# Performance work log

Hardware: AMD Instinct MI355X
Metric: run time of the kernel (lower is better)

Reference implementation:

```python
import jax, jax.numpy as jnp
import numpy as np

H = 64   # hidden_layers
D = 1    # frame_dimension
N = 2048 # n_samples (batch)
T = 512  # seq_len


def setup_inputs() -> dict:
    key = jax.random.key(0)
    ks = jax.random.split(key, 12)
    s = 1.0 / np.sqrt(H)
    u = lambda k, shape: jax.random.uniform(k, shape, jnp.float32, -s, s)
    return {
        "y": jax.random.normal(ks[0], (N, T), dtype=jnp.float32),
        "W_ih1": u(ks[1], (4 * H, D)),
        "W_hh1": u(ks[2], (4 * H, H)),
        "b_ih1": u(ks[3], (4 * H,)),
        "b_hh1": u(ks[4], (4 * H,)),
        "W_ih2": u(ks[5], (4 * H, H)),
        "W_hh2": u(ks[6], (4 * H, H)),
        "b_ih2": u(ks[7], (4 * H,)),
        "b_hh2": u(ks[8], (4 * H,)),
        "W_lin": u(ks[9], (D, H)),
        "b_lin": u(ks[10], (D,)),
        "pre_output_len": 1,
    }


def _lstm_cell(x, h, c, W_ih, W_hh, b_ih, b_hh):
    # gates in PyTorch LSTMCell order: input, forget, cell(g), output
    g = x @ W_ih.T + b_ih + h @ W_hh.T + b_hh  # [n, 4H]
    i, f, gg, o = jnp.split(g, 4, axis=-1)
    i = jax.nn.sigmoid(i)
    f = jax.nn.sigmoid(f)
    gg = jnp.tanh(gg)
    o = jax.nn.sigmoid(o)
    c2 = f * c + i * gg
    h2 = o * jnp.tanh(c2)
    return h2, c2


def reference(y, W_ih1, W_hh1, b_ih1, b_hh1, W_ih2, W_hh2, b_ih2, b_hh2,
              W_lin, b_lin, pre_output_len):
    n = y.shape[0]
    zeros = jnp.zeros((n, H), dtype=jnp.float32)
    init = (zeros, zeros, zeros, zeros)

    def step(carry, x_t):
        h1, c1, h2, c2 = carry
        h1, c1 = _lstm_cell(x_t, h1, c1, W_ih1, W_hh1, b_ih1, b_hh1)
        h2, c2 = _lstm_cell(h1, h2, c2, W_ih2, W_hh2, b_ih2, b_hh2)
        out = h2 @ W_lin.T + b_lin  # [n, D]
        return (h1, c1, h2, c2), out

    ys = jnp.swapaxes(y, 0, 1)[:, :, None]  # [T, n, 1]
    _, outs = jax.lax.scan(step, init, ys)  # [T, n, D]
    outs = outs[pre_output_len:]            # drop first pre_output_len steps (static)
    # torch.cat along dim=1 of [n, D] chunks -> [n, (T - pre)*D]
    return jnp.transpose(outs, (1, 0, 2)).reshape(n, -1)
```

## Files before the change

### kernel.cpp

```cpp
#include <hip/hip_runtime.h>


typedef __attribute__((ext_vector_type(8))) short short8;
typedef __attribute__((ext_vector_type(4))) float f32x4;

#define XPITCH 2060
#define XP 0
#define HP 32960
#define OPR 51392
#define LDS_BYTES 84160
#define PLANE(layer, buf, hl) (HP + ((((layer) * 2 + (buf)) * 2) + (hl)) * 2304)

__device__ __forceinline__ float fast_rcp(float x) { return __builtin_amdgcn_rcpf(x); }
__device__ __forceinline__ float sigm(float x) { return fast_rcp(1.0f + __expf(-x)); }
__device__ __forceinline__ float tanh2(float x) {
  const float e = __expf(-2.0f * x);
  return fmaf(2.0f, fast_rcp(1.0f + e), -1.0f);
}
__device__ __forceinline__ unsigned short bf_rne(float f) {
  unsigned u = __float_as_uint(f);
  return (unsigned short)((u + 0x7FFFu + ((u >> 16) & 1u)) >> 16);
}
__device__ __forceinline__ void split8(const float* p, short8& hi, short8& lo) {
#pragma unroll
  for (int e = 0; e < 8; ++e) {
    float v = p[e];
    unsigned short h = bf_rne(v);
    float hf = __uint_as_float(((unsigned)h) << 16);
    hi[e] = (short)h;
    lo[e] = (short)bf_rne(v - hf);
  }
}
__device__ __forceinline__ unsigned cvt_pk(float a, float b) {
  unsigned r;
  asm("v_cvt_pk_bf16_f32 %0, %1, %2" : "=v"(r) : "v"(a), "v"(b));
  return r;
}
__device__ __forceinline__ f32x4 mfma16(short8 a, short8 b, f32x4 c) {
  return __builtin_amdgcn_mfma_f32_16x16x32_bf16(a, b, c, 0, 0, 0);
}

__global__ __launch_bounds__(512, 2) void lstm2_pipe(
    const float* __restrict__ y, const float* __restrict__ Wih1,
    const float* __restrict__ Whh1, const float* __restrict__ bih1,
    const float* __restrict__ bhh1, const float* __restrict__ Wih2,
    const float* __restrict__ Whh2, const float* __restrict__ bih2,
    const float* __restrict__ bhh2, const float* __restrict__ Wlin,
    const float* __restrict__ blin, float* __restrict__ out) {
  extern __shared__ char smem[];
  const int tid = threadIdx.x;
  const int w = tid >> 6;
  const int lane = tid & 63;
  const int g = lane >> 4;
  const int s = lane & 15;
  const int s0 = blockIdx.x * 16;

  for (int i = tid; i < 16 * 512; i += 512) {
    const int ss = i >> 9, t = i & 511;
    *(float*)(smem + XP + ss * XPITCH + t * 4) = y[(size_t)(s0 + ss) * 512 + t];
  }
  for (int i = tid; i < 18432 / 4; i += 512) *(float*)(smem + HP + i * 4) = 0.f;

  const float bl0 = blin[0];
  __syncthreads();

  if (w < 4) {
    short8 a1h[4][2], a1l[4][2];
    {
      const int row = 16 * w + s;
#pragma unroll
      for (int p = 0; p < 4; ++p)
#pragma unroll
        for (int c = 0; c < 2; ++c)
          split8(Whh1 + (size_t)(p * 64 + row) * 64 + 32 * c + 8 * g, a1h[p][c], a1l[p][c]);
    }
    float bias1c[4][4], wih1c[4][4];
#pragma unroll
    for (int p = 0; p < 4; ++p)
#pragma unroll
      for (int r = 0; r < 4; ++r) {
        const int row = p * 64 + 16 * w + 4 * g + r;
        bias1c[p][r] = bih1[row] + bhh1[row];
        wih1c[p][r] = Wih1[row];
      }
    float c1[4] = {0.f, 0.f, 0.f, 0.f};
    const int boffc0 = s * 144 + 16 * g;
    const int hoff = s * 144 + 32 * w + 8 * g;

#pragma unroll 1
    for (int k = 0; k <= 512; ++k) {
      if (k < 512) {
        const int rbuf = (k - 1) & 1;
        const int wbuf = k & 1;
        const float x = *(const float*)(smem + XP + s * XPITCH + k * 4);
        f32x4 acc[4];
#pragma unroll
        for (int p = 0; p < 4; ++p)
#pragma unroll
          for (int r = 0; r < 4; ++r) acc[p][r] = fmaf(wih1c[p][r], x, bias1c[p][r]);
#pragma unroll
        for (int c = 0; c < 2; ++c) {
          const int boff = boffc0 + 64 * c;
          const short8 Bh = *(const short8*)(smem + PLANE(0, rbuf, 0) + boff);
          const short8 Bl = *(const short8*)(smem + PLANE(0, rbuf, 1) + boff);
#pragma unroll
          for (int p = 0; p < 4; ++p) acc[p] = mfma16(a1h[p][c], Bh, acc[p]);
#pragma unroll
          for (int p = 0; p < 4; ++p) acc[p] = mfma16(a1h[p][c], Bl, acc[p]);
#pragma unroll
          for (int p = 0; p < 4; ++p) acc[p] = mfma16(a1l[p][c], Bh, acc[p]);
        }
        float h1n[4];
#pragma unroll
        for (int r = 0; r < 4; ++r) {
          const float ig = sigm(acc[0][r]), fg = sigm(acc[1][r]);
          const float gg = tanh2(acc[2][r]), og = sigm(acc[3][r]);
          c1[r] = fmaf(fg, c1[r], ig * gg);
          h1n[r] = og * tanh2(c1[r]);
        }
        const unsigned hA = cvt_pk(h1n[0], h1n[1]), hB = cvt_pk(h1n[2], h1n[3]);
        const unsigned lA = cvt_pk(h1n[0] - __uint_as_float(hA << 16),
                                   h1n[1] - __uint_as_float(hA & 0xFFFF0000u));
        const unsigned lB = cvt_pk(h1n[2] - __uint_as_float(hB << 16),
                                   h1n[3] - __uint_as_float(hB & 0xFFFF0000u));
        *(uint2*)(smem + PLANE(0, wbuf, 0) + hoff) = make_uint2(hA, hB);
        *(uint2*)(smem + PLANE(0, wbuf, 1) + hoff) = make_uint2(lA, lB);
      }
      __syncthreads();
    }
  } else {
    const int ow = w - 4;
    short8 a2h[4][4], a2l[4][4];
    {
      const int row = 16 * ow + s;
#pragma unroll
      for (int p = 0; p < 4; ++p)
#pragma unroll
        for (int c = 0; c < 4; ++c) {
          const float* src = (c < 2) ? (Wih2 + (size_t)(p * 64 + row) * 64 + 32 * c + 8 * g)
                                     : (Whh2 + (size_t)(p * 64 + row) * 64 + 32 * (c - 2) + 8 * g);
          split8(src, a2h[p][c], a2l[p][c]);
        }
    }
    float bias2c[4][4], wlinc[4];
#pragma unroll
    for (int p = 0; p < 4; ++p)
#pragma unroll
      for (int r = 0; r < 4; ++r) {
        const int row = p * 64 + 16 * ow + 4 * g + r;
        bias2c[p][r] = bih2[row] + bhh2[row];
      }
#pragma unroll
    for (int r = 0; r < 4; ++r) wlinc[r] = Wlin[16 * ow + 4 * g + r];
    float c2[4] = {0.f, 0.f, 0.f, 0.f};
    const int boffc0 = s * 144 + 16 * g;
    const int hoff = s * 144 + 32 * ow + 8 * g;

#pragma unroll 1
    for (int k = 0; k <= 512; ++k) {
      if (k >= 66 && ((k - 2) & 63) == 0) {
        const int base = k - 66;
        const int thr = ow * 64 + lane;
        const int ss = thr & 15, grp = thr >> 4;
#pragma unroll
        for (int q = 0; q < 4; ++q) {
          const int idx = base + grp * 4 + q;
          const int slot = idx & 127;
          const char* op = smem + OPR + slot * 256 + ss * 4;
          const float v = *(const float*)(op) + *(const float*)(op + 64) +
                          *(const float*)(op + 128) + *(const float*)(op + 192) + bl0;
          out[(size_t)(s0 + ss) * 511 + idx] = v;
        }
      }
      if (k >= 1) {
        const int t2 = k - 1;
        const int h1buf = (k - 1) & 1;
        const int h2rbuf = k & 1;
        const int h2wbuf = (k - 1) & 1;
        f32x4 acc[4];
#pragma unroll
        for (int p = 0; p < 4; ++p)
#pragma unroll
          for (int r = 0; r < 4; ++r) acc[p][r] = bias2c[p][r];
#pragma unroll
        for (int c = 0; c < 4; ++c) {
          const int lay = (c < 2) ? 0 : 1;
          const int buf = (c < 2) ? h1buf : h2rbuf;
          const int boff = boffc0 + 64 * (c & 1);
          const short8 Bh = *(const short8*)(smem + PLANE(lay, buf, 0) + boff);
          const short8 Bl = *(const short8*)(smem + PLANE(lay, buf, 1) + boff);
#pragma unroll
          for (int p = 0; p < 4; ++p) acc[p] = mfma16(a2h[p][c], Bh, acc[p]);
#pragma unroll
          for (int p = 0; p < 4; ++p) acc[p] = mfma16(a2h[p][c], Bl, acc[p]);
#pragma unroll
          for (int p = 0; p < 4; ++p) acc[p] = mfma16(a2l[p][c], Bh, acc[p]);
        }
        float h2n[4];
#pragma unroll
        for (int r = 0; r < 4; ++r) {
          const float ig = sigm(acc[0][r]), fg = sigm(acc[1][r]);
          const float gg = tanh2(acc[2][r]), og = sigm(acc[3][r]);
          c2[r] = fmaf(fg, c2[r], ig * gg);
          h2n[r] = og * tanh2(c2[r]);
        }
        const unsigned hA = cvt_pk(h2n[0], h2n[1]), hB = cvt_pk(h2n[2], h2n[3]);
        const unsigned lA = cvt_pk(h2n[0] - __uint_as_float(hA << 16),
                                   h2n[1] - __uint_as_float(hA & 0xFFFF0000u));
        const unsigned lB = cvt_pk(h2n[2] - __uint_as_float(hB << 16),
                                   h2n[3] - __uint_as_float(hB & 0xFFFF0000u));
        *(uint2*)(smem + PLANE(1, h2wbuf, 0) + hoff) = make_uint2(hA, hB);
        *(uint2*)(smem + PLANE(1, h2wbuf, 1) + hoff) = make_uint2(lA, lB);

        if (t2 >= 1) {
          float pw = wlinc[0] * h2n[0];
          pw = fmaf(wlinc[1], h2n[1], pw);
          pw = fmaf(wlinc[2], h2n[2], pw);
          pw = fmaf(wlinc[3], h2n[3], pw);
          pw += __shfl_xor(pw, 16, 64);
          pw += __shfl_xor(pw, 32, 64);
          if (g == 0)
            *(float*)(smem + OPR + ((t2 - 1) & 127) * 256 + ow * 64 + s * 4) = pw;
        }
      }
      __syncthreads();
    }
    {
      const int thr = ow * 64 + lane;
      for (int e = thr; e < 63 * 16; e += 256) {
        const int ss = e & 15, off = e >> 4;
        const int idx = 448 + off;
        const int slot = idx & 127;
        const char* op = smem + OPR + slot * 256 + ss * 4;
        const float v = *(const float*)(op) + *(const float*)(op + 64) +
                        *(const float*)(op + 128) + *(const float*)(op + 192) + bl0;
        out[(size_t)(s0 + ss) * 511 + idx] = v;
      }
    }
  }
}

extern "C" void kernel_launch(void* const* d_in, const int* in_sizes, int n_in,
                              void* d_out, int out_size, void* d_ws, size_t ws_size,
                              hipStream_t stream) {
  const float* y    = (const float*)d_in[0];
  const float* Wih1 = (const float*)d_in[1];
  const float* Whh1 = (const float*)d_in[2];
  const float* bih1 = (const float*)d_in[3];
  const float* bhh1 = (const float*)d_in[4];
  const float* Wih2 = (const float*)d_in[5];
  const float* Whh2 = (const float*)d_in[6];
  const float* bih2 = (const float*)d_in[7];
  const float* bhh2 = (const float*)d_in[8];
  const float* Wlin = (const float*)d_in[9];
  const float* blin = (const float*)d_in[10];
  float* out = (float*)d_out;

  hipFuncSetAttribute((const void*)lstm2_pipe,
                      hipFuncAttributeMaxDynamicSharedMemorySize, LDS_BYTES);
  lstm2_pipe<<<dim3(128), dim3(512), LDS_BYTES, stream>>>(
      y, Wih1, Whh1, bih1, bhh1, Wih2, Whh2, bih2, bhh2, Wlin, blin, out);
}
```

Baseline: 648.0 us.

## Replace block barriers with LDS flag counters and 4-slot ring for layer decoupling

Replaces the per-step __syncthreads between layer-1 and layer-2 wavegroups with per-wave progress counters in LDS and spin-waits. Hidden states go into a 4-slot ring, so layer 1 can run up to three steps ahead of layer 2. It also splits the MFMA chains into two independent accumulators to shorten dependency latency, raises priority around the MFMA block, and fuses the gate math into fewer exp/rcp calls. The cost is more LDS, spin-wait polling overhead, and the risk of memory-ordering bugs in the flag protocol.

```diff
diff --git a/kernel.cpp b/kernel.cpp
--- a/kernel.cpp
+++ b/kernel.cpp
@@ -4,19 +4,16 @@
 typedef __attribute__((ext_vector_type(8))) short short8;
 typedef __attribute__((ext_vector_type(4))) float f32x4;
 
+#define NT 512
 #define XPITCH 2060
 #define XP 0
 #define HP 32960
-#define OPR 51392
-#define LDS_BYTES 84160
-#define PLANE(layer, buf, hl) (HP + ((((layer) * 2 + (buf)) * 2) + (hl)) * 2304)
+#define RING 69824
+#define FLG 102592
+#define LDS_BYTES 102720
+#define PLANE(layer, slot, hl) (HP + ((((layer) * 4 + (slot)) * 2) + (hl)) * 2304)
 
 __device__ __forceinline__ float fast_rcp(float x) { return __builtin_amdgcn_rcpf(x); }
-__device__ __forceinline__ float sigm(float x) { return fast_rcp(1.0f + __expf(-x)); }
-__device__ __forceinline__ float tanh2(float x) {
-  const float e = __expf(-2.0f * x);
-  return fmaf(2.0f, fast_rcp(1.0f + e), -1.0f);
-}
 __device__ __forceinline__ unsigned short bf_rne(float f) {
   unsigned u = __float_as_uint(f);
   return (unsigned short)((u + 0x7FFFu + ((u >> 16) & 1u)) >> 16);
@@ -39,8 +36,25 @@
 __device__ __forceinline__ f32x4 mfma16(short8 a, short8 b, f32x4 c) {
   return __builtin_amdgcn_mfma_f32_16x16x32_bf16(a, b, c, 0, 0, 0);
 }
-
-__global__ __launch_bounds__(512, 2) void lstm2_pipe(
+__device__ __forceinline__ void cell(float i, float f, float gg, float o,
+                                     float& c, float& h) {
+  const float ei = __expf(-i), ef = __expf(-f), eg = __expf(-2.f * gg),
+              eo = __expf(-o);
+  const float P = (1.f - eg) * fast_rcp((1.f + ei) * (1.f + eg));
+  c = fmaf(c, fast_rcp(1.f + ef), P);
+  const float cc = fminf(15.f, fmaxf(-15.f, c));
+  const float ec = __expf(-2.f * cc);
+  h = (1.f - ec) * fast_rcp((1.f + eo) * (1.f + ec));
+}
+__device__ __forceinline__ void wait_min_ge(const volatile int* c4, int need) {
+  while (true) {
+    const int m = min(min(c4[0], c4[1]), min(c4[2], c4[3]));
+    if (m >= need) return;
+    __builtin_amdgcn_s_sleep(1);
+  }
+}
+
+__global__ __launch_bounds__(512, 2) void lstm2_async(
     const float* __restrict__ y, const float* __restrict__ Wih1,
     const float* __restrict__ Whh1, const float* __restrict__ bih1,
     const float* __restrict__ bhh1, const float* __restrict__ Wih2,
@@ -59,21 +73,22 @@
     const int ss = i >> 9, t = i & 511;
     *(float*)(smem + XP + ss * XPITCH + t * 4) = y[(size_t)(s0 + ss) * 512 + t];
   }
-  for (int i = tid; i < 18432 / 4; i += 512) *(float*)(smem + HP + i * 4) = 0.f;
-
-  const float bl0 = blin[0];
+  for (int i = tid; i < 36864 / 4; i += 512) *(float*)(smem + HP + i * 4) = 0.f;
+  if (tid < 8) *(volatile int*)(smem + FLG + tid * 4) = -1;
   __syncthreads();
+
+  volatile int* cE = (volatile int*)(smem + FLG);
+  volatile int* cO = (volatile int*)(smem + FLG + 16);
+  const int bo0 = s * 144 + 16 * g, bo1 = bo0 + 64;
 
   if (w < 4) {
     short8 a1h[4][2], a1l[4][2];
-    {
-      const int row = 16 * w + s;
-#pragma unroll
-      for (int p = 0; p < 4; ++p)
-#pragma unroll
-        for (int c = 0; c < 2; ++c)
-          split8(Whh1 + (size_t)(p * 64 + row) * 64 + 32 * c + 8 * g, a1h[p][c], a1l[p][c]);
-    }
+#pragma unroll
+    for (int p = 0; p < 4; ++p)
+#pragma unroll
+      for (int c = 0; c < 2; ++c)
+        split8(Whh1 + (size_t)(p * 64 + 16 * w + s) * 64 + 32 * c + 8 * g,
+               a1h[p][c], a1l[p][c]);
     float bias1c[4][4], wih1c[4][4];
 #pragma unroll
     for (int p = 0; p < 4; ++p)
@@ -84,157 +99,183 @@
         wih1c[p][r] = Wih1[row];
       }
     float c1[4] = {0.f, 0.f, 0.f, 0.f};
-    const int boffc0 = s * 144 + 16 * g;
-    const int hoff = s * 144 + 32 * w + 8 * g;
+    const int hwr0 = s * 144 + 32 * w + 8 * g;
 
 #pragma unroll 1
-    for (int k = 0; k <= 512; ++k) {
-      if (k < 512) {
-        const int rbuf = (k - 1) & 1;
-        const int wbuf = k & 1;
-        const float x = *(const float*)(smem + XP + s * XPITCH + k * 4);
-        f32x4 acc[4];
-#pragma unroll
-        for (int p = 0; p < 4; ++p)
-#pragma unroll
-          for (int r = 0; r < 4; ++r) acc[p][r] = fmaf(wih1c[p][r], x, bias1c[p][r]);
-#pragma unroll
-        for (int c = 0; c < 2; ++c) {
-          const int boff = boffc0 + 64 * c;
-          const short8 Bh = *(const short8*)(smem + PLANE(0, rbuf, 0) + boff);
-          const short8 Bl = *(const short8*)(smem + PLANE(0, rbuf, 1) + boff);
-#pragma unroll
-          for (int p = 0; p < 4; ++p) acc[p] = mfma16(a1h[p][c], Bh, acc[p]);
-#pragma unroll
-          for (int p = 0; p < 4; ++p) acc[p] = mfma16(a1h[p][c], Bl, acc[p]);
-#pragma unroll
-          for (int p = 0; p < 4; ++p) acc[p] = mfma16(a1l[p][c], Bh, acc[p]);
-        }
-        float h1n[4];
-#pragma unroll
-        for (int r = 0; r < 4; ++r) {
-          const float ig = sigm(acc[0][r]), fg = sigm(acc[1][r]);
-          const float gg = tanh2(acc[2][r]), og = sigm(acc[3][r]);
-          c1[r] = fmaf(fg, c1[r], ig * gg);
-          h1n[r] = og * tanh2(c1[r]);
-        }
-        const unsigned hA = cvt_pk(h1n[0], h1n[1]), hB = cvt_pk(h1n[2], h1n[3]);
-        const unsigned lA = cvt_pk(h1n[0] - __uint_as_float(hA << 16),
-                                   h1n[1] - __uint_as_float(hA & 0xFFFF0000u));
-        const unsigned lB = cvt_pk(h1n[2] - __uint_as_float(hB << 16),
-                                   h1n[3] - __uint_as_float(hB & 0xFFFF0000u));
-        *(uint2*)(smem + PLANE(0, wbuf, 0) + hoff) = make_uint2(hA, hB);
-        *(uint2*)(smem + PLANE(0, wbuf, 1) + hoff) = make_uint2(lA, lB);
-      }
-      __syncthreads();
+    for (int k = 0; k < NT; ++k) {
+      if (k >= 1) wait_min_ge(cE, k - 1);
+      if (k >= 4) wait_min_ge(cO, k - 4);
+      asm volatile("" ::: "memory");
+      const int rp0 = PLANE(0, (k - 1) & 3, 0), rp1 = PLANE(0, (k - 1) & 3, 1);
+      const short8 Bh0 = *(const short8*)(smem + rp0 + bo0);
+      const short8 Bl0 = *(const short8*)(smem + rp1 + bo0);
+      const short8 Bh1 = *(const short8*)(smem + rp0 + bo1);
+      const short8 Bl1 = *(const short8*)(smem + rp1 + bo1);
+      const float x = *(const float*)(smem + XP + s * XPITCH + k * 4);
+      f32x4 acc[4], acx[4];
+#pragma unroll
+      for (int p = 0; p < 4; ++p) {
+#pragma unroll
+        for (int r = 0; r < 4; ++r) acc[p][r] = fmaf(wih1c[p][r], x, bias1c[p][r]);
+        acx[p] = (f32x4){0.f, 0.f, 0.f, 0.f};
+      }
+      __builtin_amdgcn_s_setprio(1);
+#pragma unroll
+      for (int p = 0; p < 4; ++p) acc[p] = mfma16(a1h[p][0], Bh0, acc[p]);
+#pragma unroll
+      for (int p = 0; p < 4; ++p) acx[p] = mfma16(a1h[p][1], Bh1, acx[p]);
+#pragma unroll
+      for (int p = 0; p < 4; ++p) acc[p] = mfma16(a1h[p][0], Bl0, acc[p]);
+#pragma unroll
+      for (int p = 0; p < 4; ++p) acx[p] = mfma16(a1h[p][1], Bl1, acx[p]);
+#pragma unroll
+      for (int p = 0; p < 4; ++p) acc[p] = mfma16(a1l[p][0], Bh0, acc[p]);
+#pragma unroll
+      for (int p = 0; p < 4; ++p) acx[p] = mfma16(a1l[p][1], Bh1, acx[p]);
+      __builtin_amdgcn_s_setprio(0);
+#pragma unroll
+      for (int p = 0; p < 4; ++p) acc[p] += acx[p];
+
+      float h1n[4];
+#pragma unroll
+      for (int r = 0; r < 4; ++r)
+        cell(acc[0][r], acc[1][r], acc[2][r], acc[3][r], c1[r], h1n[r]);
+      const unsigned hA = cvt_pk(h1n[0], h1n[1]), hB = cvt_pk(h1n[2], h1n[3]);
+      const unsigned lA = cvt_pk(h1n[0] - __uint_as_float(hA << 16),
+                                 h1n[1] - __uint_as_float(hA & 0xFFFF0000u));
+      const unsigned lB = cvt_pk(h1n[2] - __uint_as_float(hB << 16),
+                                 h1n[3] - __uint_as_float(hB & 0xFFFF0000u));
+      *(uint2*)(smem + PLANE(0, k & 3, 0) + hwr0) = make_uint2(hA, hB);
+      *(uint2*)(smem + PLANE(0, k & 3, 1) + hwr0) = make_uint2(lA, lB);
+      asm volatile("s_waitcnt lgkmcnt(0)" ::: "memory");
+      if (lane == 0) cE[w] = k;
     }
   } else {
     const int ow = w - 4;
     short8 a2h[4][4], a2l[4][4];
-    {
-      const int row = 16 * ow + s;
-#pragma unroll
-      for (int p = 0; p < 4; ++p)
-#pragma unroll
-        for (int c = 0; c < 4; ++c) {
-          const float* src = (c < 2) ? (Wih2 + (size_t)(p * 64 + row) * 64 + 32 * c + 8 * g)
-                                     : (Whh2 + (size_t)(p * 64 + row) * 64 + 32 * (c - 2) + 8 * g);
-          split8(src, a2h[p][c], a2l[p][c]);
-        }
-    }
+#pragma unroll
+    for (int p = 0; p < 4; ++p)
+#pragma unroll
+      for (int c = 0; c < 4; ++c) {
+        const float* src = (c < 2) ? (Wih2 + (size_t)(p * 64 + 16 * ow + s) * 64 + 32 * c + 8 * g)
+                                   : (Whh2 + (size_t)(p * 64 + 16 * ow + s) * 64 + 32 * (c - 2) + 8 * g);
+        split8(src, a2h[p][c], a2l[p][c]);
+      }
     float bias2c[4][4], wlinc[4];
 #pragma unroll
     for (int p = 0; p < 4; ++p)
 #pragma unroll
-      for (int r = 0; r < 4; ++r) {
-        const int row = p * 64 + 16 * ow + 4 * g + r;
-        bias2c[p][r] = bih2[row] + bhh2[row];
-      }
+      for (int r = 0; r < 4; ++r)
+        bias2c[p][r] = bih2[p * 64 + 16 * ow + 4 * g + r] +
+                       bhh2[p * 64 + 16 * ow + 4 * g + r];
 #pragma unroll
     for (int r = 0; r < 4; ++r) wlinc[r] = Wlin[16 * ow + 4 * g + r];
+    const float bl0 = blin[0];
     float c2[4] = {0.f, 0.f, 0.f, 0.f};
-    const int boffc0 = s * 144 + 16 * g;
-    const int hoff = s * 144 + 32 * ow + 8 * g;
+    const int hwr0 = s * 144 + 32 * ow + 8 * g;
 
 #pragma unroll 1
-    for (int k = 0; k <= 512; ++k) {
-      if (k >= 66 && ((k - 2) & 63) == 0) {
-        const int base = k - 66;
+    for (int j = 0; j < NT; ++j) {
+      wait_min_ge(cE, j);
+      if (j >= 1) wait_min_ge(cO, j - 1);
+      asm volatile("" ::: "memory");
+
+      if (j >= 66 && ((j - 2) & 63) == 0) {
+        const int base = j - 66;
         const int thr = ow * 64 + lane;
-        const int ss = thr & 15, grp = thr >> 4;
+        const int ss2 = thr & 15, grp = thr >> 4;
 #pragma unroll
         for (int q = 0; q < 4; ++q) {
           const int idx = base + grp * 4 + q;
-          const int slot = idx & 127;
-          const char* op = smem + OPR + slot * 256 + ss * 4;
+          const char* op = smem + RING + (idx & 127) * 256 + ss2 * 4;
           const float v = *(const float*)(op) + *(const float*)(op + 64) +
                           *(const float*)(op + 128) + *(const float*)(op + 192) + bl0;
-          out[(size_t)(s0 + ss) * 511 + idx] = v;
+          out[(size_t)(s0 + ss2) * 511 + idx] = v;
         }
       }
-      if (k >= 1) {
-        const int t2 = k - 1;
-        const int h1buf = (k - 1) & 1;
-        const int h2rbuf = k & 1;
-        const int h2wbuf = (k - 1) & 1;
-        f32x4 acc[4];
-#pragma unroll
-        for (int p = 0; p < 4; ++p)
-#pragma unroll
-          for (int r = 0; r < 4; ++r) acc[p][r] = bias2c[p][r];
-#pragma unroll
-        for (int c = 0; c < 4; ++c) {
-          const int lay = (c < 2) ? 0 : 1;
-          const int buf = (c < 2) ? h1buf : h2rbuf;
-          const int boff = boffc0 + 64 * (c & 1);
-          const short8 Bh = *(const short8*)(smem + PLANE(lay, buf, 0) + boff);
-          const short8 Bl = *(const short8*)(smem + PLANE(lay, buf, 1) + boff);
-#pragma unroll
-          for (int p = 0; p < 4; ++p) acc[p] = mfma16(a2h[p][c], Bh, acc[p]);
-#pragma unroll
-          for (int p = 0; p < 4; ++p) acc[p] = mfma16(a2h[p][c], Bl, acc[p]);
-#pragma unroll
-          for (int p = 0; p < 4; ++p) acc[p] = mfma16(a2l[p][c], Bh, acc[p]);
-        }
-        float h2n[4];
-#pragma unroll
-        for (int r = 0; r < 4; ++r) {
-          const float ig = sigm(acc[0][r]), fg = sigm(acc[1][r]);
-          const float gg = tanh2(acc[2][r]), og = sigm(acc[3][r]);
-          c2[r] = fmaf(fg, c2[r], ig * gg);
-          h2n[r] = og * tanh2(c2[r]);
-        }
-        const unsigned hA = cvt_pk(h2n[0], h2n[1]), hB = cvt_pk(h2n[2], h2n[3]);
-        const unsigned lA = cvt_pk(h2n[0] - __uint_as_float(hA << 16),
-                                   h2n[1] - __uint_as_float(hA & 0xFFFF0000u));
-        const unsigned lB = cvt_pk(h2n[2] - __uint_as_float(hB << 16),
-                                   h2n[3] - __uint_as_float(hB & 0xFFFF0000u));
-        *(uint2*)(smem + PLANE(1, h2wbuf, 0) + hoff) = make_uint2(hA, hB);
-        *(uint2*)(smem + PLANE(1, h2wbuf, 1) + hoff) = make_uint2(lA, lB);
-
-        if (t2 >= 1) {
-          float pw = wlinc[0] * h2n[0];
-          pw = fmaf(wlinc[1], h2n[1], pw);
-          pw = fmaf(wlinc[2], h2n[2], pw);
-          pw = fmaf(wlinc[3], h2n[3], pw);
-          pw += __shfl_xor(pw, 16, 64);
-          pw += __shfl_xor(pw, 32, 64);
-          if (g == 0)
-            *(float*)(smem + OPR + ((t2 - 1) & 127) * 256 + ow * 64 + s * 4) = pw;
-        }
-      }
-      __syncthreads();
+
+      const int rp0 = PLANE(0, j & 3, 0), rp1 = PLANE(0, j & 3, 1);
+      const int rq0 = PLANE(1, (j - 1) & 3, 0), rq1 = PLANE(1, (j - 1) & 3, 1);
+      const short8 Bh0 = *(const short8*)(smem + rp0 + bo0);
+      const short8 Bl0 = *(const short8*)(smem + rp1 + bo0);
+      const short8 Bh1 = *(const short8*)(smem + rp0 + bo1);
+      const short8 Bl1 = *(const short8*)(smem + rp1 + bo1);
+      const short8 Ch0 = *(const short8*)(smem + rq0 + bo0);
+      const short8 Cl0 = *(const short8*)(smem + rq1 + bo0);
+      const short8 Ch1 = *(const short8*)(smem + rq0 + bo1);
+      const short8 Cl1 = *(const short8*)(smem + rq1 + bo1);
+      f32x4 acc[4], acx[4];
+#pragma unroll
+      for (int p = 0; p < 4; ++p) {
+        acc[p] = (f32x4){bias2c[p][0], bias2c[p][1], bias2c[p][2], bias2c[p][3]};
+        acx[p] = (f32x4){0.f, 0.f, 0.f, 0.f};
+      }
+      __builtin_amdgcn_s_setprio(1);
+#pragma unroll
+      for (int p = 0; p < 4; ++p) acc[p] = mfma16(a2h[p][0], Bh0, acc[p]);
+#pragma unroll
+      for (int p = 0; p < 4; ++p) acx[p] = mfma16(a2h[p][1], Bh1, acx[p]);
+#pragma unroll
+      for (int p = 0; p < 4; ++p) acc[p] = mfma16(a2h[p][0], Bl0, acc[p]);
+#pragma unroll
+      for (int p = 0; p < 4; ++p) acx[p] = mfma16(a2h[p][1], Bl1, acx[p]);
+#pragma unroll
+      for (int p = 0; p < 4; ++p) acc[p] = mfma16(a2l[p][0], Bh0, acc[p]);
+#pragma unroll
+      for (int p = 0; p < 4; ++p) acx[p] = mfma16(a2l[p][1], Bh1, acx[p]);
+#pragma unroll
+      for (int p = 0; p < 4; ++p) acc[p] = mfma16(a2h[p][2], Ch0, acc[p]);
+#pragma unroll
+      for (int p = 0; p < 4; ++p) acx[p] = mfma16(a2h[p][3], Ch1, acx[p]);
+#pragma unroll
+      for (int p = 0; p < 4; ++p) acc[p] = mfma16(a2h[p][2], Cl0, acc[p]);
+#pragma unroll
+      for (int p = 0; p < 4; ++p) acx[p] = mfma16(a2h[p][3], Cl1, acx[p]);
+#pragma unroll
+      for (int p = 0; p < 4; ++p) acc[p] = mfma16(a2l[p][2], Ch0, acc[p]);
+#pragma unroll
+      for (int p = 0; p < 4; ++p) acx[p] = mfma16(a2l[p][3], Ch1, acx[p]);
+      __builtin_amdgcn_s_setprio(0);
+#pragma unroll
+      for (int p = 0; p < 4; ++p) acc[p] += acx[p];
+
+      float h2n[4];
+#pragma unroll
+      for (int r = 0; r < 4; ++r)
+        cell(acc[0][r], acc[1][r], acc[2][r], acc[3][r], c2[r], h2n[r]);
+      const unsigned hA = cvt_pk(h2n[0], h2n[1]), hB = cvt_pk(h2n[2], h2n[3]);
+      const unsigned lA = cvt_pk(h2n[0] - __uint_as_float(hA << 16),
+                                 h2n[1] - __uint_as_float(hA & 0xFFFF0000u));
+      const unsigned lB = cvt_pk(h2n[2] - __uint_as_float(hB << 16),
+                                 h2n[3] - __uint_as_float(hB & 0xFFFF0000u));
+      *(uint2*)(smem + PLANE(1, j & 3, 0) + hwr0) = make_uint2(hA, hB);
+      *(uint2*)(smem + PLANE(1, j & 3, 1) + hwr0) = make_uint2(lA, lB);
+
+      if (j >= 1) {
+        float pw = wlinc[0] * h2n[0];
+        pw = fmaf(wlinc[1], h2n[1], pw);
+        pw = fmaf(wlinc[2], h2n[2], pw);
+        pw = fmaf(wlinc[3], h2n[3], pw);
+        pw += __shfl_xor(pw, 16, 64);
+        pw += __shfl_xor(pw, 32, 64);
+        if (g == 0)
+          *(float*)(smem + RING + ((j - 1) & 127) * 256 + ow * 64 + s * 4) = pw;
+      }
+      asm volatile("s_waitcnt lgkmcnt(0)" ::: "memory");
+      if (lane == 0) cO[ow] = j;
     }
+
+    wait_min_ge(cO, NT - 1);
+    asm volatile("" ::: "memory");
     {
       const int thr = ow * 64 + lane;
       for (int e = thr; e < 63 * 16; e += 256) {
-        const int ss = e & 15, off = e >> 4;
+        const int ss2 = e & 15, off = e >> 4;
         const int idx = 448 + off;
-        const int slot = idx & 127;
-        const char* op = smem + OPR + slot * 256 + ss * 4;
+        const char* op = smem + RING + (idx & 127) * 256 + ss2 * 4;
         const float v = *(const float*)(op) + *(const float*)(op + 64) +
                         *(const float*)(op + 128) + *(const float*)(op + 192) + bl0;
-        out[(size_t)(s0 + ss) * 511 + idx] = v;
+        out[(size_t)(s0 + ss2) * 511 + idx] = v;
       }
     }
   }
@@ -256,8 +297,8 @@
   const float* blin = (const float*)d_in[10];
   float* out = (float*)d_out;
 
-  hipFuncSetAttribute((const void*)lstm2_pipe,
+  hipFuncSetAttribute((const void*)lstm2_async,
                       hipFuncAttributeMaxDynamicSharedMemorySize, LDS_BYTES);
-  lstm2_pipe<<<dim3(128), dim3(512), LDS_BYTES, stream>>>(
+  lstm2_async<<<dim3(128), dim3(512), LDS_BYTES, stream>>>(
       y, Wih1, Whh1, bih1, bhh1, Wih2, Whh2, bih2, bhh2, Wlin, blin, out);
 }
```

Measured after the change: 794.9 us. 22.7% more time.
